# Performance work log

Measured on AMD Instinct MI355X. Metric: run time of the kernel, lower is better.

## Reference

```python
import jax, jax.numpy as jnp
import numpy as np

SMALL = 1e-7
EPS = 1e-6


def setup_inputs() -> dict:
    key = jax.random.key(0)
    k1, k2 = jax.random.split(key)
    B, C, h, w = 8, 3, 1024, 1024
    src = jax.random.normal(k1, (B, C, h, w), dtype=jnp.float32)
    # near-identity homographies so warped coords land mostly in-bounds
    H = jnp.eye(3, dtype=jnp.float32)[None] + 0.05 * jax.random.normal(k2, (B, 3, 3), dtype=jnp.float32)
    return {"src": src, "H": H}


def reference(src, H):
    B, C, h, w = src.shape
    # homogeneous pixel grid: (3, h, w) = [x, y, 1]
    xx = jnp.arange(w, dtype=jnp.float32)
    yy = jnp.arange(h, dtype=jnp.float32)
    gx, gy = jnp.meshgrid(xx, yy)  # (h, w) each
    grid = jnp.stack([gx, gy, jnp.ones_like(gx)], axis=0)  # (3, h, w)

    # per-pixel homography transform: (B,3,h,w)
    warped = jnp.einsum('bij,jhw->bihw', H, grid)
    T = warped[:, 2]  # (B,h,w)
    T = T + EPS * (1.0 - (jnp.abs(T) >= SMALL).astype(jnp.float32))
    x = warped[:, 0] / T  # (B,h,w) source x-coords
    y = warped[:, 1] / T  # (B,h,w) source y-coords

    # bilinear sample with clamped corner indices (matches torch impl)
    x0 = jnp.floor(x).astype(jnp.int32)
    y0 = jnp.floor(y).astype(jnp.int32)
    x1 = jnp.clip(x0 + 1, 0, w - 1)
    y1 = jnp.clip(y0 + 1, 0, h - 1)
    x0 = jnp.clip(x0, 0, w - 1)
    y0 = jnp.clip(y0, 0, h - 1)

    im = jnp.transpose(src, (0, 2, 3, 1))  # (B,h,w,C)
    b = jnp.arange(B, dtype=jnp.int32)[:, None, None]  # (B,1,1)
    Ia = im[b, y0, x0]  # (B,h,w,C)
    Ib = im[b, y1, x0]
    Ic = im[b, y0, x1]
    Id = im[b, y1, x1]

    x0f, x1f = x0.astype(jnp.float32), x1.astype(jnp.float32)
    y0f, y1f = y0.astype(jnp.float32), y1.astype(jnp.float32)
    wa = ((x1f - x) * (y1f - y))[..., None]
    wb = ((x1f - x) * (y - y0f))[..., None]
    wc = ((x - x0f) * (y1f - y))[..., None]
    wd = ((x - x0f) * (y - y0f))[..., None]

    out = wa * Ia + wb * Ib + wc * Ic + wd * Id  # (B,h,w,C)
    return jnp.transpose(out, (0, 3, 1, 2))  # (B,C,h,w)
```

## Files before the change

kernel.cpp:

```cpp
#include <hip/hip_runtime.h>
#include <math.h>
#include <limits.h>
#include <string.h>


#define SMALL_F 1e-7f
#define EPS_F   1e-6f
#define PX 4

__device__ __forceinline__ int cvt_f32_i32_x86(float f) {
    if (f >= 2147483648.0f) return INT_MIN;
    return (int)f;
}

__global__ void __launch_bounds__(256)
warp_bilinear_kernel(const float* __restrict__ src, const float* __restrict__ Hm,
                     float* __restrict__ out, int B, int h, int w) {
#pragma clang fp contract(off)
    const int y  = blockIdx.y;
    const int b  = blockIdx.z;
    const int tx = threadIdx.x;
    const int xstart = blockIdx.x * (256 * PX) + tx;

    const float* Hb = Hm + (size_t)b * 9;
    const float H0 = Hb[0], H1 = Hb[1], H2 = Hb[2];
    const float H3 = Hb[3], H4 = Hb[4], H5 = Hb[5];
    const float H6 = Hb[6], H7 = Hb[7], H8 = Hb[8];
    const float gy = (float)y;
    const float p1 = H1 * gy, p4 = H4 * gy, p7 = H7 * gy;

    int   idx0[PX], idx1[PX];
    float wav[PX], wbv[PX], wcv[PX], wdv[PX];
    bool  sA[PX], sC[PX], valid[PX];

#pragma unroll
    for (int k = 0; k < PX; ++k) {
        int x = xstart + 256 * k;
        valid[k] = (x < w);
        float gx = (float)x;
        float w0 = (H0 * gx + p1) + H2;
        float w1 = (H3 * gx + p4) + H5;
        float T  = (H6 * gx + p7) + H8;
        if (!(fabsf(T) >= SMALL_F)) T = T + EPS_F;
        float xs = w0 / T;
        float ys = w1 / T;
        float fx = floorf(xs), fy = floorf(ys);
        int x0u = cvt_f32_i32_x86(fx);
        int y0u = cvt_f32_i32_x86(fy);
        int x1 = min(max(x0u + 1, 0), w - 1);
        int y1 = min(max(y0u + 1, 0), h - 1);
        int x0 = min(max(x0u, 0), w - 1);
        int y0 = min(max(y0u, 0), h - 1);
        float t1 = (float)x1 - xs;
        float t2 = (float)y1 - ys;
        float t3 = ys - (float)y0;
        float t4 = xs - (float)x0;
        wav[k] = t1 * t2;
        wbv[k] = t1 * t3;
        wcv[k] = t4 * t2;
        wdv[k] = t4 * t3;
        int xb = min(max(x0u, 0), w - 2);
        sA[k] = (x0 == xb);
        sC[k] = (x1 == xb);
        idx0[k] = y0 * w + xb;
        idx1[k] = y1 * w + xb;
    }

    const size_t plane = (size_t)h * (size_t)w;
    const float* sb = src + (size_t)b * 3 * plane;
    float* ob = out + (size_t)b * 3 * plane + (size_t)y * (size_t)w;

#pragma unroll
    for (int c = 0; c < 3; ++c) {
        const float* sc = sb + (size_t)c * plane;
        float* oc = ob + (size_t)c * plane;
#pragma unroll
        for (int k = 0; k < PX; ++k) {
            if (!valid[k]) continue;
            float pr0[2], pr1[2];
            __builtin_memcpy(pr0, sc + idx0[k], 8);
            __builtin_memcpy(pr1, sc + idx1[k], 8);
            float Ia = sA[k] ? pr0[0] : pr0[1];
            float Ic = sC[k] ? pr0[0] : pr0[1];
            float Ib = sA[k] ? pr1[0] : pr1[1];
            float Id = sC[k] ? pr1[0] : pr1[1];
            float r = ((wav[k] * Ia + wbv[k] * Ib) + wcv[k] * Ic) + wdv[k] * Id;
            __builtin_nontemporal_store(r, oc + xstart + 256 * k);
        }
    }
}

extern "C" void kernel_launch(void* const* d_in, const int* in_sizes, int n_in,
                              void* d_out, int out_size, void* d_ws, size_t ws_size,
                              hipStream_t stream) {
    const float* src = (const float*)d_in[0];
    const float* Hm  = (const float*)d_in[1];
    float* out = (float*)d_out;

    const int B = in_sizes[1] / 9;
    const int C = 3;
    const size_t plane = (size_t)in_sizes[0] / ((size_t)B * C);
    const int h = 1024;
    const int w = (int)(plane / h);

    dim3 block(256, 1, 1);
    dim3 grid((w + 256 * PX - 1) / (256 * PX), h, B);
    warp_bilinear_kernel<<<grid, block, 0, stream>>>(src, Hm, out, B, h, w);
}
```

Baseline: 186.0 us.

## Batch gather loads across channels and pack bilinear math into float2 vectors

Computes coordinates and weights as float2 pairs so the compiler can use packed FP32 instructions. When all pixels of a thread are in range, it issues all 24 gather loads for the three channels up front, giving more memory-level parallelism. A wave-uniform ballot then picks a fast path with no clip selects when no lane hits the x border. The cost is higher register pressure from holding 48 loaded floats, which may reduce occupancy, plus extra code size for three paths.

```diff
diff --git a/kernel.cpp b/kernel.cpp
--- a/kernel.cpp
+++ b/kernel.cpp
@@ -7,6 +7,8 @@
 #define SMALL_F 1e-7f
 #define EPS_F   1e-6f
 #define PX 4
+
+typedef float v2f __attribute__((ext_vector_type(2)));
 
 __device__ __forceinline__ int cvt_f32_i32_x86(float f) {
     if (f >= 2147483648.0f) return INT_MIN;
@@ -29,63 +31,129 @@
     const float gy = (float)y;
     const float p1 = H1 * gy, p4 = H4 * gy, p7 = H7 * gy;
 
-    int   idx0[PX], idx1[PX];
-    float wav[PX], wbv[PX], wcv[PX], wdv[PX];
-    bool  sA[PX], sC[PX], valid[PX];
+    unsigned idx0[PX], idx1[PX];
+    v2f wa2[2], wb2[2], wc2[2], wd2[2];
+    bool sA[PX], sC[PX], valid[PX];
+    bool allvalid = true;
 
 #pragma unroll
-    for (int k = 0; k < PX; ++k) {
-        int x = xstart + 256 * k;
-        valid[k] = (x < w);
-        float gx = (float)x;
-        float w0 = (H0 * gx + p1) + H2;
-        float w1 = (H3 * gx + p4) + H5;
-        float T  = (H6 * gx + p7) + H8;
-        if (!(fabsf(T) >= SMALL_F)) T = T + EPS_F;
-        float xs = w0 / T;
-        float ys = w1 / T;
-        float fx = floorf(xs), fy = floorf(ys);
-        int x0u = cvt_f32_i32_x86(fx);
-        int y0u = cvt_f32_i32_x86(fy);
-        int x1 = min(max(x0u + 1, 0), w - 1);
-        int y1 = min(max(y0u + 1, 0), h - 1);
-        int x0 = min(max(x0u, 0), w - 1);
-        int y0 = min(max(y0u, 0), h - 1);
-        float t1 = (float)x1 - xs;
-        float t2 = (float)y1 - ys;
-        float t3 = ys - (float)y0;
-        float t4 = xs - (float)x0;
-        wav[k] = t1 * t2;
-        wbv[k] = t1 * t3;
-        wcv[k] = t4 * t2;
-        wdv[k] = t4 * t3;
-        int xb = min(max(x0u, 0), w - 2);
-        sA[k] = (x0 == xb);
-        sC[k] = (x1 == xb);
-        idx0[k] = y0 * w + xb;
-        idx1[k] = y1 * w + xb;
+    for (int j = 0; j < 2; ++j) {
+        const int ka = 2 * j, kb = 2 * j + 1;
+        const int xa = xstart + 256 * ka, xb_ = xstart + 256 * kb;
+        valid[ka] = (xa < w); valid[kb] = (xb_ < w);
+        allvalid &= valid[ka] & valid[kb];
+        v2f gx = { (float)xa, (float)xb_ };
+        v2f w0 = (H0 * gx + p1) + H2;
+        v2f w1 = (H3 * gx + p4) + H5;
+        v2f T  = (H6 * gx + p7) + H8;
+        float Ta = T[0], Tb = T[1];
+        if (!(fabsf(Ta) >= SMALL_F)) Ta = Ta + EPS_F;
+        if (!(fabsf(Tb) >= SMALL_F)) Tb = Tb + EPS_F;
+        v2f xs = { w0[0] / Ta, w0[1] / Tb };
+        v2f ys = { w1[0] / Ta, w1[1] / Tb };
+
+        v2f x0f, x1f, y0f, y1f;
+#pragma unroll
+        for (int e = 0; e < 2; ++e) {
+            const int k = 2 * j + e;
+            int x0u = cvt_f32_i32_x86(floorf(xs[e]));
+            int y0u = cvt_f32_i32_x86(floorf(ys[e]));
+            int x1 = min(max(x0u + 1, 0), w - 1);
+            int y1 = min(max(y0u + 1, 0), h - 1);
+            int x0 = min(max(x0u, 0), w - 1);
+            int y0 = min(max(y0u, 0), h - 1);
+            x0f[e] = (float)x0; x1f[e] = (float)x1;
+            y0f[e] = (float)y0; y1f[e] = (float)y1;
+            int xb = min(max(x0u, 0), w - 2);
+            sA[k] = (x0 == xb);
+            sC[k] = (x1 == xb);
+            idx0[k] = (unsigned)(y0 * w + xb);
+            idx1[k] = (unsigned)(y1 * w + xb);
+        }
+        v2f t1 = x1f - xs;
+        v2f t2 = y1f - ys;
+        v2f t3 = ys - y0f;
+        v2f t4 = xs - x0f;
+        wa2[j] = t1 * t2;
+        wb2[j] = t1 * t3;
+        wc2[j] = t4 * t2;
+        wd2[j] = t4 * t3;
     }
 
     const size_t plane = (size_t)h * (size_t)w;
     const float* sb = src + (size_t)b * 3 * plane;
     float* ob = out + (size_t)b * 3 * plane + (size_t)y * (size_t)w;
 
+    if (allvalid) {
+        float q0[3][PX][2], q1[3][PX][2];
 #pragma unroll
-    for (int c = 0; c < 3; ++c) {
-        const float* sc = sb + (size_t)c * plane;
-        float* oc = ob + (size_t)c * plane;
+        for (int c = 0; c < 3; ++c) {
+            const float* sc = sb + (size_t)c * plane;
 #pragma unroll
-        for (int k = 0; k < PX; ++k) {
-            if (!valid[k]) continue;
-            float pr0[2], pr1[2];
-            __builtin_memcpy(pr0, sc + idx0[k], 8);
-            __builtin_memcpy(pr1, sc + idx1[k], 8);
-            float Ia = sA[k] ? pr0[0] : pr0[1];
-            float Ic = sC[k] ? pr0[0] : pr0[1];
-            float Ib = sA[k] ? pr1[0] : pr1[1];
-            float Id = sC[k] ? pr1[0] : pr1[1];
-            float r = ((wav[k] * Ia + wbv[k] * Ib) + wcv[k] * Ic) + wdv[k] * Id;
-            __builtin_nontemporal_store(r, oc + xstart + 256 * k);
+            for (int k = 0; k < PX; ++k) {
+                __builtin_memcpy(q0[c][k], sc + idx0[k], 8);
+                __builtin_memcpy(q1[c][k], sc + idx1[k], 8);
+            }
+        }
+        bool noxclip = sA[0] & sA[1] & sA[2] & sA[3] &
+                       !(sC[0] | sC[1] | sC[2] | sC[3]);
+        if (__ballot(noxclip) == ~0ull) {
+#pragma unroll
+            for (int c = 0; c < 3; ++c) {
+                float* oc = ob + (size_t)c * plane;
+#pragma unroll
+                for (int j = 0; j < 2; ++j) {
+                    const int ka = 2 * j, kb = 2 * j + 1;
+                    v2f Ia = { q0[c][ka][0], q0[c][kb][0] };
+                    v2f Ic = { q0[c][ka][1], q0[c][kb][1] };
+                    v2f Ib = { q1[c][ka][0], q1[c][kb][0] };
+                    v2f Id = { q1[c][ka][1], q1[c][kb][1] };
+                    v2f r = ((wa2[j] * Ia + wb2[j] * Ib) + wc2[j] * Ic) + wd2[j] * Id;
+                    __builtin_nontemporal_store(r[0], oc + xstart + 256 * ka);
+                    __builtin_nontemporal_store(r[1], oc + xstart + 256 * kb);
+                }
+            }
+        } else {
+#pragma unroll
+            for (int c = 0; c < 3; ++c) {
+                float* oc = ob + (size_t)c * plane;
+#pragma unroll
+                for (int j = 0; j < 2; ++j) {
+                    const int ka = 2 * j, kb = 2 * j + 1;
+                    v2f Ia = { sA[ka] ? q0[c][ka][0] : q0[c][ka][1],
+                               sA[kb] ? q0[c][kb][0] : q0[c][kb][1] };
+                    v2f Ic = { sC[ka] ? q0[c][ka][0] : q0[c][ka][1],
+                               sC[kb] ? q0[c][kb][0] : q0[c][kb][1] };
+                    v2f Ib = { sA[ka] ? q1[c][ka][0] : q1[c][ka][1],
+                               sA[kb] ? q1[c][kb][0] : q1[c][kb][1] };
+                    v2f Id = { sC[ka] ? q1[c][ka][0] : q1[c][ka][1],
+                               sC[kb] ? q1[c][kb][0] : q1[c][kb][1] };
+                    v2f r = ((wa2[j] * Ia + wb2[j] * Ib) + wc2[j] * Ic) + wd2[j] * Id;
+                    __builtin_nontemporal_store(r[0], oc + xstart + 256 * ka);
+                    __builtin_nontemporal_store(r[1], oc + xstart + 256 * kb);
+                }
+            }
+        }
+    } else {
+#pragma unroll
+        for (int c = 0; c < 3; ++c) {
+            const float* sc = sb + (size_t)c * plane;
+            float* oc = ob + (size_t)c * plane;
+#pragma unroll
+            for (int k = 0; k < PX; ++k) {
+                if (!valid[k]) continue;
+                float pr0[2], pr1[2];
+                __builtin_memcpy(pr0, sc + idx0[k], 8);
+                __builtin_memcpy(pr1, sc + idx1[k], 8);
+                float Ia = sA[k] ? pr0[0] : pr0[1];
+                float Ic = sC[k] ? pr0[0] : pr0[1];
+                float Ib = sA[k] ? pr1[0] : pr1[1];
+                float Id = sC[k] ? pr1[0] : pr1[1];
+                const int j = k >> 1, e = k & 1;
+                float r = ((wa2[j][e] * Ia + wb2[j][e] * Ib) + wc2[j][e] * Ic)
+                          + wd2[j][e] * Id;
+                __builtin_nontemporal_store(r, oc + xstart + 256 * k);
+            }
         }
     }
 }
```

Result: no change. 182.8 us (median of 2 runs) (-1.7%).
